# Kernel optimization log

Measured on AMD Instinct MI355X. Metric: run time of the kernel, lower is better.

## Reference

```python
import jax, jax.numpy as jnp
import numpy as np

B, CI, CO, K, SD, H, W = 8, 128, 128, 3, 512, 256, 256


def setup_inputs() -> dict:
    key = jax.random.key(0)
    k0, k1, k2, k3 = jax.random.split(key, 4)
    x = jax.random.normal(k0, (B, CI, H, W), jnp.float32)
    style = jax.random.normal(k1, (B, SD), jnp.float32)
    # learned params
    w_base = jax.random.normal(k2, (1, CO, CI, K, K), jnp.float32)   # ModulatedConv2d.weight
    aff_w = jax.random.normal(k3, (CI, SD), jnp.float32)             # affine weight [out=CI, in=SD]
    aff_b = jnp.ones((CI,), jnp.float32)                             # bias_init=1
    return {"x": x, "style": style, "w_base": w_base, "aff_w": aff_w, "aff_b": aff_b}


def reference(x, style, w_base, aff_w, aff_b):
    b, ci, h, w_ = x.shape
    co, k = w_base.shape[1], w_base.shape[3]
    # affine: FullyConnectedLayer, linear activation, weight_gain = 1/sqrt(style_dim)
    aff_gain = 1.0 / np.sqrt(aff_w.shape[1])
    s = style @ (aff_w * aff_gain).T + aff_b                 # [B, CI]
    # modulate
    wgain = 1.0 / np.sqrt(ci * k * k)
    wt = w_base * wgain * s[:, None, :, None, None]          # [B, CO, CI, K, K]
    # demodulate
    d = jax.lax.rsqrt(jnp.sum(wt * wt, axis=(2, 3, 4)) + 1e-8)  # [B, CO]
    wt = wt * d[:, :, None, None, None]
    # grouped conv, groups = batch, padding = k//2 (up=down=1 path)
    wt = wt.reshape(b * co, ci, k, k)
    xg = x.reshape(1, b * ci, h, w_)
    pad = k // 2
    y = jax.lax.conv_general_dilated(
        xg, wt, window_strides=(1, 1), padding=[(pad, pad), (pad, pad)],
        dimension_numbers=("NCHW", "OIHW", "NCHW"), feature_group_count=b)
    return y.reshape(b, co, h, w_)
```

## Files before the change

kernel.cpp:

```cpp
#include <hip/hip_runtime.h>
#include <stdint.h>

#define BB 8
#define SD 512

typedef unsigned short u16;
typedef __attribute__((ext_vector_type(8))) __bf16 bf16x8;
typedef __attribute__((ext_vector_type(4))) float f32x4;

__device__ float g_s[BB * 128];
__device__ u16 g_wtb[BB * 9 * 2 * 8192];
__device__ u16 g_xb[(size_t)BB * 258 * 258 * 128 + 2048];

typedef const __attribute__((address_space(1))) uint32_t* gp1;
typedef __attribute__((address_space(3))) uint32_t* lp3;

__device__ __forceinline__ void glds16(const void* g, void* l) {
    __builtin_amdgcn_global_load_lds((gp1)g, (lp3)l, 16, 0, 0);
}
__device__ __forceinline__ void glds4(const void* g, void* l) {
    __builtin_amdgcn_global_load_lds((gp1)g, (lp3)l, 4, 0, 0);
}

__device__ __forceinline__ u16 f2bf(float f) {
    uint32_t u = __float_as_uint(f);
    u += 0x7FFFu + ((u >> 16) & 1u);
    return (u16)(u >> 16);
}

__global__ void affine_kernel(const float* __restrict__ style,
                              const float* __restrict__ aff_w,
                              const float* __restrict__ aff_b) {
    int b = blockIdx.x;
    int ci = threadIdx.x;
    const float gain = 0.044194173824159216f;
    const float* st = style + b * SD;
    const float* aw = aff_w + ci * SD;
    float acc = 0.f;
    #pragma unroll 8
    for (int j = 0; j < SD; ++j) acc += st[j] * aw[j];
    g_s[b * 128 + ci] = acc * gain + aff_b[ci];
}

__global__ __launch_bounds__(256) void modulate_kernel(const float* __restrict__ w_base) {
    int blk = blockIdx.x;
    int b = blk >> 7, co = blk & 127;
    int tid = threadIdx.x;
    const float wgain = 0.029462782549439483f;
    const int n = 1152;
    const float* wb = w_base + co * n;
    const float* sp = g_s + b * 128;

    float v[5];
    float sq = 0.f;
    #pragma unroll
    for (int i = 0; i < 5; ++i) {
        int idx = tid + i * 256;
        float w = 0.f;
        if (idx < n) {
            int ci = idx / 9;
            w = wb[idx] * wgain * sp[ci];
        }
        v[i] = w;
        sq += w * w;
    }
    #pragma unroll
    for (int off = 32; off > 0; off >>= 1) sq += __shfl_down(sq, off, 64);
    __shared__ float red[4];
    int lane = tid & 63, wvi = tid >> 6;
    if (lane == 0) red[wvi] = sq;
    __syncthreads();
    float tot = red[0] + red[1] + red[2] + red[3];
    float d = rsqrtf(tot + 1e-8f);
    #pragma unroll
    for (int i = 0; i < 5; ++i) {
        int idx = tid + i * 256;
        if (idx < n) {
            int ci = idx / 9;
            int k9 = idx - ci * 9;
            u16 hv = f2bf(v[i] * d);
            int ci64 = ci & 63;
            size_t base = ((size_t)(b * 9 + k9) * 2 + (ci >> 6)) * 8192;
            g_wtb[base + co * 64 + (ci64 ^ ((co & 7) << 3))] = hv;
        }
    }
}

__global__ __launch_bounds__(256) void zero_border_kernel() {
    int b = blockIdx.x;
    uint4 z = make_uint4(0, 0, 0, 0);
    char* xbB = (char*)g_xb;
    for (int i = threadIdx.x; i < 16448; i += 256) {
        size_t pix; int k;
        if (i < 4128)       { pix = (size_t)(b * 258 + 0)   * 258 + (i >> 4);            k = i & 15; }
        else if (i < 8256)  { int j = i - 4128;  pix = (size_t)(b * 258 + 257) * 258 + (j >> 4);       k = j & 15; }
        else if (i < 12352) { int j = i - 8256;  pix = (size_t)(b * 258 + 1 + (j >> 4)) * 258 + 0;     k = j & 15; }
        else                { int j = i - 12352; pix = (size_t)(b * 258 + 1 + (j >> 4)) * 258 + 257;   k = j & 15; }
        *(uint4*)(xbB + pix * 256 + (size_t)k * 16) = z;
    }
}

__global__ __launch_bounds__(256) void transpose_kernel(const float* __restrict__ x) {
    __shared__ __align__(16) u16 t_lds[64 * 128];
    const int chunk = blockIdx.x;
    const int gy = blockIdx.y;
    const int b = blockIdx.z;
    const int px0 = chunk * 64;
    const int tid = threadIdx.x;
    const int l = tid & 63;
    const int g = tid >> 6;
    const int key = (l + 1) & 7;
    const int px = px0 + l;

    const float* xb_ = x + (size_t)b * 128 * 65536 + (size_t)gy * 256 + px;
    char* ldsB = (char*)t_lds;

    #pragma unroll
    for (int cc = 0; cc < 4; ++cc) {
        int c = g + cc * 4;
        uint32_t dw[4];
        #pragma unroll
        for (int dgrp = 0; dgrp < 4; ++dgrp) {
            float lo = xb_[(size_t)(c * 8 + dgrp * 2) * 65536];
            float hi = xb_[(size_t)(c * 8 + dgrp * 2 + 1) * 65536];
            dw[dgrp] = (uint32_t)f2bf(lo) | ((uint32_t)f2bf(hi) << 16);
        }
        int slot = c ^ key;
        *(uint4*)(ldsB + l * 256 + slot * 16) = *(uint4*)dw;
    }
    __syncthreads();

    char* outB = (char*)g_xb;
    #pragma unroll
    for (int it = 0; it < 4; ++it) {
        int flat = it * 256 + tid;
        int r = flat >> 4, k = flat & 15;
        size_t pix = ((size_t)(b * 258 + gy + 1)) * 258 + (px0 + r + 1);
        *(uint4*)(outB + pix * 256 + k * 16) = *(const uint4*)(ldsB + r * 256 + k * 16);
    }
}

__global__ __launch_bounds__(512, 2) void conv_kernel(float* __restrict__ y) {
    __shared__ __align__(16) u16 xs[18 * 18 * 128];
    __shared__ __align__(16) u16 ab[2][8192];

    const int b = blockIdx.y;
    const int t = blockIdx.x;
    const int swzt = (t & 7) * 32 + (t >> 3);
    const int ty = swzt >> 4, tx = swzt & 15;
    const int y0 = ty * 16, x0 = tx * 16;
    const int tid = threadIdx.x;
    const int lane = tid & 63, wv = tid >> 6;
    const int kgrp = lane >> 4, lp = lane & 15;
    const int coBase = (wv & 1) * 64;
    const int py0w = (wv >> 1) * 4;

    const char* xbB = (const char*)g_xb;
    const char* wtbB = (const char*)(g_wtb) + (size_t)b * 294912;
    char* xsB = (char*)xs;

    for (int i = wv; i < 108; i += 8) {
        int row = i / 6, sub = i - row * 6;
        size_t rb = ((size_t)(b * 258 + y0 + row) * 258 + x0) * 256;
        char* dst = xsB + row * 4608;
        if (sub < 4) glds16(xbB + rb + sub * 1024 + lane * 16, dst + sub * 1024);
        else {
            int px = 12 + sub;
            glds4(xbB + rb + px * 256 + lane * 4, dst + px * 256);
        }
    }
    #pragma unroll
    for (int q = 0; q < 2; ++q) {
        int j = wv * 2 + q;
        glds16(wtbB + j * 1024 + lane * 16, (char*)ab[0] + j * 1024);
    }
    __syncthreads();

    f32x4 acc[4][4];
    #pragma unroll
    for (int mf = 0; mf < 4; ++mf)
        #pragma unroll
        for (int nf = 0; nf < 4; ++nf)
            acc[mf][nf] = (f32x4){0.f, 0.f, 0.f, 0.f};

    const int aswz = (lp & 7) << 4;
    const int abase = (coBase + lp) * 128;

    for (int s = 0; s < 18; ++s) {
        if (s < 17) {
            const char* src = wtbB + (s + 1) * 16384;
            char* dst = (char*)ab[(s + 1) & 1];
            #pragma unroll
            for (int q = 0; q < 2; ++q) {
                int j = wv * 2 + q;
                glds16(src + j * 1024 + lane * 16, dst + j * 1024);
            }
        }

        const int tap = s >> 1, chunk = s & 1;
        const int ky = tap / 3, kx = tap - ky * 3;
        const char* abuf = (const char*)ab[s & 1];
        const int ccol = lp + kx;
        const int bswz = (ccol & 7) << 4;
        const int brow0 = (py0w + ky) * 4608 + ccol * 256;
        const int cb0 = chunk * 128;

        #pragma unroll
        for (int ks = 0; ks < 2; ++ks) {
            const int ka = (ks * 64 + kgrp * 16) ^ aswz;
            const int kb = (cb0 + ks * 64 + kgrp * 16) ^ bswz;
            bf16x8 af[4];
            #pragma unroll
            for (int mf = 0; mf < 4; ++mf)
                af[mf] = *(const bf16x8*)(abuf + abase + mf * 2048 + ka);
            bf16x8 bfv[4];
            #pragma unroll
            for (int nf = 0; nf < 4; ++nf)
                bfv[nf] = *(const bf16x8*)(xsB + brow0 + nf * 4608 + kb);
            #pragma unroll
            for (int mf = 0; mf < 4; ++mf)
                #pragma unroll
                for (int nf = 0; nf < 4; ++nf)
                    acc[mf][nf] = __builtin_amdgcn_mfma_f32_16x16x32_bf16(
                        af[mf], bfv[nf], acc[mf][nf], 0, 0, 0);
        }
        __syncthreads();
    }

    float* yb = y + (size_t)b * 128 * 65536;
    #pragma unroll
    for (int mf = 0; mf < 4; ++mf) {
        #pragma unroll
        for (int nf = 0; nf < 4; ++nf) {
            int gy = y0 + py0w + nf;
            #pragma unroll
            for (int r = 0; r < 4; ++r) {
                int co = coBase + mf * 16 + kgrp * 4 + r;
                yb[(size_t)co * 65536 + gy * 256 + x0 + lp] = acc[mf][nf][r];
            }
        }
    }
}

extern "C" void kernel_launch(void* const* d_in, const int* in_sizes, int n_in,
                              void* d_out, int out_size, void* d_ws, size_t ws_size,
                              hipStream_t stream) {
    const float* x = (const float*)d_in[0];
    const float* style = (const float*)d_in[1];
    const float* w_base = (const float*)d_in[2];
    const float* aff_w = (const float*)d_in[3];
    const float* aff_b = (const float*)d_in[4];
    float* y = (float*)d_out;

    affine_kernel<<<BB, 128, 0, stream>>>(style, aff_w, aff_b);
    modulate_kernel<<<BB * 128, 256, 0, stream>>>(w_base);
    zero_border_kernel<<<BB, 256, 0, stream>>>();
    transpose_kernel<<<dim3(4, 256, BB), 256, 0, stream>>>(x);
    conv_kernel<<<dim3(256, BB), 512, 0, stream>>>(y);
}
```

Before: 369.2 us.

## Split conv input tile into channel halves to raise occupancy; vectorize transpose loads

```diff
diff --git a/kernel.cpp b/kernel.cpp
--- a/kernel.cpp
+++ b/kernel.cpp
@@ -107,26 +107,30 @@
     const int b = blockIdx.z;
     const int px0 = chunk * 64;
     const int tid = threadIdx.x;
-    const int l = tid & 63;
-    const int g = tid >> 6;
-    const int key = (l + 1) & 7;
-    const int px = px0 + l;
-
-    const float* xb_ = x + (size_t)b * 128 * 65536 + (size_t)gy * 256 + px;
+    const int pq = tid & 15;
+    const int cig = tid >> 4;
+
+    const float* base = x + (size_t)b * 128 * 65536 + (size_t)gy * 256 + px0 + pq * 4;
     char* ldsB = (char*)t_lds;
 
-    #pragma unroll
-    for (int cc = 0; cc < 4; ++cc) {
-        int c = g + cc * 4;
+    float4 v[8];
+    #pragma unroll
+    for (int c = 0; c < 8; ++c)
+        v[c] = *(const float4*)(base + (size_t)(cig * 8 + c) * 65536);
+
+    #pragma unroll
+    for (int j = 0; j < 4; ++j) {
         uint32_t dw[4];
         #pragma unroll
-        for (int dgrp = 0; dgrp < 4; ++dgrp) {
-            float lo = xb_[(size_t)(c * 8 + dgrp * 2) * 65536];
-            float hi = xb_[(size_t)(c * 8 + dgrp * 2 + 1) * 65536];
-            dw[dgrp] = (uint32_t)f2bf(lo) | ((uint32_t)f2bf(hi) << 16);
-        }
-        int slot = c ^ key;
-        *(uint4*)(ldsB + l * 256 + slot * 16) = *(uint4*)dw;
+        for (int d = 0; d < 4; ++d) {
+            const float* lo4 = (const float*)&v[2 * d];
+            const float* hi4 = (const float*)&v[2 * d + 1];
+            dw[d] = (uint32_t)f2bf(lo4[j]) | ((uint32_t)f2bf(hi4[j]) << 16);
+        }
+        int px = pq * 4 + j;
+        int key = (px0 + px + 1) & 7;
+        int slot = cig ^ key;
+        *(uint4*)(ldsB + px * 256 + slot * 16) = *(uint4*)dw;
     }
     __syncthreads();
 
@@ -140,8 +144,8 @@
     }
 }
 
-__global__ __launch_bounds__(512, 2) void conv_kernel(float* __restrict__ y) {
-    __shared__ __align__(16) u16 xs[18 * 18 * 128];
+__global__ __launch_bounds__(512, 4) void conv_kernel(float* __restrict__ y) {
+    __shared__ __align__(16) u16 xs[18 * 18 * 64];
     __shared__ __align__(16) u16 ab[2][8192];
 
     const int b = blockIdx.y;
@@ -159,23 +163,6 @@
     const char* wtbB = (const char*)(g_wtb) + (size_t)b * 294912;
     char* xsB = (char*)xs;
 
-    for (int i = wv; i < 108; i += 8) {
-        int row = i / 6, sub = i - row * 6;
-        size_t rb = ((size_t)(b * 258 + y0 + row) * 258 + x0) * 256;
-        char* dst = xsB + row * 4608;
-        if (sub < 4) glds16(xbB + rb + sub * 1024 + lane * 16, dst + sub * 1024);
-        else {
-            int px = 12 + sub;
-            glds4(xbB + rb + px * 256 + lane * 4, dst + px * 256);
-        }
-    }
-    #pragma unroll
-    for (int q = 0; q < 2; ++q) {
-        int j = wv * 2 + q;
-        glds16(wtbB + j * 1024 + lane * 16, (char*)ab[0] + j * 1024);
-    }
-    __syncthreads();
-
     f32x4 acc[4][4];
     #pragma unroll
     for (int mf = 0; mf < 4; ++mf)
@@ -186,45 +173,72 @@
     const int aswz = (lp & 7) << 4;
     const int abase = (coBase + lp) * 128;
 
-    for (int s = 0; s < 18; ++s) {
-        if (s < 17) {
-            const char* src = wtbB + (s + 1) * 16384;
-            char* dst = (char*)ab[(s + 1) & 1];
+    int s = 0;
+    for (int h = 0; h < 2; ++h) {
+        for (int i = wv; i < 54; i += 8) {
+            int row = i / 3, sub = i - row * 3;
+            size_t rb = ((size_t)(b * 258 + y0 + row) * 258 + x0) * 256 + h * 128;
+            char* dst = xsB + row * 2304;
+            if (sub < 2) {
+                glds16(xbB + rb + (size_t)(sub * 8 + (lane >> 3)) * 256 + (lane & 7) * 16,
+                       dst + sub * 1024);
+            } else {
+                glds4(xbB + rb + (size_t)(16 + (lane >> 5)) * 256 + (lane & 31) * 4,
+                      dst + 2048);
+            }
+        }
+        if (h == 0) {
             #pragma unroll
             for (int q = 0; q < 2; ++q) {
                 int j = wv * 2 + q;
-                glds16(src + j * 1024 + lane * 16, dst + j * 1024);
-            }
-        }
-
-        const int tap = s >> 1, chunk = s & 1;
-        const int ky = tap / 3, kx = tap - ky * 3;
-        const char* abuf = (const char*)ab[s & 1];
-        const int ccol = lp + kx;
-        const int bswz = (ccol & 7) << 4;
-        const int brow0 = (py0w + ky) * 4608 + ccol * 256;
-        const int cb0 = chunk * 128;
-
-        #pragma unroll
-        for (int ks = 0; ks < 2; ++ks) {
-            const int ka = (ks * 64 + kgrp * 16) ^ aswz;
-            const int kb = (cb0 + ks * 64 + kgrp * 16) ^ bswz;
-            bf16x8 af[4];
+                glds16(wtbB + j * 1024 + lane * 16, (char*)ab[0] + j * 1024);
+            }
+        }
+        __syncthreads();
+
+        for (int tap = 0; tap < 9; ++tap, ++s) {
+            if (s < 17) {
+                int ns = s + 1;
+                int ntap = (ns >= 9) ? (ns - 9) : ns;
+                int nh = (ns >= 9) ? 1 : h;
+                const char* src = wtbB + (ntap * 2 + nh) * 16384;
+                char* dst = (char*)ab[ns & 1];
+                #pragma unroll
+                for (int q = 0; q < 2; ++q) {
+                    int j = wv * 2 + q;
+                    glds16(src + j * 1024 + lane * 16, dst + j * 1024);
+                }
+            }
+
+            const int ky = tap / 3, kx = tap - ky * 3;
+            const char* abuf = (const char*)ab[s & 1];
+            const int ccol = lp + kx;
+            const int bswz = (ccol & 7) << 4;
+            const int brow0 = ((py0w + ky) * 18 + ccol) * 128;
+
             #pragma unroll
-            for (int mf = 0; mf < 4; ++mf)
-                af[mf] = *(const bf16x8*)(abuf + abase + mf * 2048 + ka);
-            bf16x8 bfv[4];
-            #pragma unroll
-            for (int nf = 0; nf < 4; ++nf)
-                bfv[nf] = *(const bf16x8*)(xsB + brow0 + nf * 4608 + kb);
-            #pragma unroll
-            for (int mf = 0; mf < 4; ++mf)
+            for (int ks = 0; ks < 2; ++ks) {
+                const int ka = (ks * 64 + kgrp * 16) ^ aswz;
+                const int kb = (ks * 64 + kgrp * 16) ^ bswz;
+                bf16x8 af[4];
+                #pragma unroll
+                for (int mf = 0; mf < 4; ++mf)
+                    af[mf] = *(const bf16x8*)(abuf + abase + mf * 2048 + ka);
+                bf16x8 bfv[4];
                 #pragma unroll
                 for (int nf = 0; nf < 4; ++nf)
-                    acc[mf][nf] = __builtin_amdgcn_mfma_f32_16x16x32_bf16(
-                        af[mf], bfv[nf], acc[mf][nf], 0, 0, 0);
-        }
-        __syncthreads();
+                    bfv[nf] = *(const bf16x8*)(xsB + brow0 + nf * 18 * 128 + kb);
+                __builtin_amdgcn_s_setprio(1);
+                #pragma unroll
+                for (int mf = 0; mf < 4; ++mf)
+                    #pragma unroll
+                    for (int nf = 0; nf < 4; ++nf)
+                        acc[mf][nf] = __builtin_amdgcn_mfma_f32_16x16x32_bf16(
+                            af[mf], bfv[nf], acc[mf][nf], 0, 0, 0);
+                __builtin_amdgcn_s_setprio(0);
+            }
+            __syncthreads();
+        }
     }
 
     float* yb = y + (size_t)b * 128 * 65536;
```

After: 380.7 us. 1.03x slower.
